# Optimization experiments

Hardware: AMD Instinct MI355X
Metric: run time of the kernel (lower is better)

The kernel has to match this reference:

```python
import jax, jax.numpy as jnp
import numpy as np

B, M, V, TOPK = 64, 8192, 128, 64
EPS = 1e-8  # stands in for LOG_EPS and F.cosine_similarity eps clamp


def setup_inputs() -> dict:
    key = jax.random.key(0)
    k1, k2 = jax.random.split(key)
    stdev = 1.0 / np.sqrt(M + V)
    memory = jax.random.uniform(k1, (B, M, V), dtype=jnp.float32, minval=-stdev, maxval=stdev)
    v = jax.random.normal(k2, (B, V), dtype=jnp.float32)
    return {"memory": memory, "v": v, "topk": TOPK}


def reference(memory, v, topk):
    # --- similarity(v, topk): cosine similarity of query against each memory slot ---
    a = memory + EPS                      # (B, M, V)
    b = v + EPS                           # (B, V)
    num = jnp.einsum('bmv,bv->bm', a, b)  # (B, M)
    denom = jnp.maximum(
        jnp.linalg.norm(a, axis=-1) * jnp.linalg.norm(b, axis=-1)[:, None], EPS
    )
    sim = num / denom                     # (B, M), unnormalized addressing weights
    # topk masking: torch zeroes the (M - topk) smallest entries via scatter_;
    # equivalently keep values >= the topk-th largest value (ties negligible for floats)
    kth = jax.lax.top_k(sim, topk)[0][:, -1:]   # (B, 1)
    w = jnp.where(sim >= kth, sim, jnp.zeros((), sim.dtype))
    # --- write(w, v): rank-1 outer-product update ---
    new_mem = memory + w[:, :, None] * v[:, None, :]   # (B, M, V)
    # --- read(w): weighted sum over slots; torch returns (B,1,1,V) via double unsqueeze ---
    read = jnp.einsum('bm,bmv->bv', w, new_mem)[:, None, None, :]
    return read
```

## Files before the change

### kernel.cpp

```cpp
#include <hip/hip_runtime.h>
#include <hip/hip_bf16.h>

#define B_DIM 64
#define M_DIM 8192
#define V_DIM 128
#define EPS 1e-8f
#define KCAP 2048

__global__ void sim_kernel(const float* __restrict__ mem,
                           const float* __restrict__ v,
                           float* __restrict__ sim) {
    const int b   = blockIdx.y;
    const int m0  = blockIdx.x * 32;
    const int tid = threadIdx.x;

    __shared__ float vs[V_DIM];
    __shared__ float s_bn;

    if (tid < V_DIM) vs[tid] = v[b * V_DIM + tid] + EPS;
    __syncthreads();

    if (tid < 32) {
        float s = 0.f;
#pragma unroll
        for (int j = 0; j < 4; ++j) { float x = vs[tid + 32 * j]; s += x * x; }
#pragma unroll
        for (int mk = 16; mk; mk >>= 1) s += __shfl_xor(s, mk, 32);
        if (tid == 0) s_bn = sqrtf(s);
    }
    __syncthreads();

    const int r    = tid >> 5;
    const int lane = tid & 31;
    const int c    = lane * 4;
    const float bn = s_bn;

#pragma unroll
    for (int rt = 0; rt < 4; ++rt) {
        const int m = m0 + rt * 8 + r;
        const float4* rowp =
            reinterpret_cast<const float4*>(mem + ((size_t)b * M_DIM + m) * V_DIM);
        float4 x = rowp[lane];
        float a0 = x.x + EPS, a1 = x.y + EPS, a2 = x.z + EPS, a3 = x.w + EPS;
        float dot = a0 * vs[c] + a1 * vs[c + 1] + a2 * vs[c + 2] + a3 * vs[c + 3];
        float ss  = a0 * a0 + a1 * a1 + a2 * a2 + a3 * a3;
#pragma unroll
        for (int mk = 16; mk; mk >>= 1) {
            dot += __shfl_xor(dot, mk, 32);
            ss  += __shfl_xor(ss,  mk, 32);
        }
        if (lane == 0) {
            float denom = fmaxf(sqrtf(ss) * bn, EPS);
            sim[(size_t)b * M_DIM + m] = dot / denom;
        }
    }
}

__device__ __forceinline__ unsigned int f2key(float f) {
    unsigned int u = __float_as_uint(f);
    return (u & 0x80000000u) ? ~u : (u | 0x80000000u);
}
__device__ __forceinline__ float key2f(unsigned int k) {
    return (k & 0x80000000u) ? __uint_as_float(k & 0x7FFFFFFFu)
                             : __uint_as_float(~k);
}

__global__ void topk_read_kernel(const float* __restrict__ mem,
                                 const float* __restrict__ v,
                                 const float* __restrict__ sim,
                                 const int* __restrict__ topk_p,
                                 float* __restrict__ out) {
    const int b   = blockIdx.x;
    const int tid = threadIdx.x;
    const int NT  = 256;

    __shared__ unsigned int keys[M_DIM];
    __shared__ unsigned int hist[256];
    __shared__ unsigned int s_prefix;
    __shared__ int s_k;
    __shared__ int s_cnt;
    __shared__ int   s_idx[KCAP];
    __shared__ float s_w[KCAP];
    __shared__ float s_sumw2;
    __shared__ float s_acc[256];

    for (int i = tid; i < M_DIM; i += NT)
        keys[i] = f2key(sim[(size_t)b * M_DIM + i]);
    if (tid == 0) { s_prefix = 0u; s_k = topk_p[0]; s_cnt = 0; }
    __syncthreads();

    for (int p = 3; p >= 0; --p) {
        hist[tid & 255] = 0u;
        __syncthreads();
        const unsigned int dm = (p == 3) ? 0u : (0xFFFFFFFFu << ((p + 1) * 8));
        const unsigned int pf = s_prefix;
        for (int i = tid; i < M_DIM; i += NT) {
            unsigned int ky = keys[i];
            if ((ky & dm) == pf)
                atomicAdd(&hist[(ky >> (p * 8)) & 0xFFu], 1u);
        }
        __syncthreads();
        if (tid == 0) {
            int k = s_k;
            for (int vq = 255; vq >= 0; --vq) {
                int c = (int)hist[vq];
                if (k <= c) {
                    s_prefix = pf | ((unsigned int)vq << (p * 8));
                    s_k = k;
                    break;
                }
                k -= c;
            }
        }
        __syncthreads();
    }
    const unsigned int kth = s_prefix;

    for (int i = tid; i < M_DIM; i += NT) {
        unsigned int ky = keys[i];
        if (ky >= kth) {
            int pos = atomicAdd(&s_cnt, 1);
            if (pos < KCAP) { s_idx[pos] = i; s_w[pos] = key2f(ky); }
        }
    }
    __syncthreads();
    const int cnt = min(s_cnt, KCAP);

    if (tid < 64) {
        float s = 0.f;
        for (int i = tid; i < cnt; i += 64) s += s_w[i] * s_w[i];
#pragma unroll
        for (int mk = 32; mk; mk >>= 1) s += __shfl_xor(s, mk, 64);
        if (tid == 0) s_sumw2 = s;
    }
    __syncthreads();

    const int col  = tid & 127;
    const int half = tid >> 7;
    float acc = 0.f;
    const float* mb = mem + (size_t)b * M_DIM * V_DIM;
    for (int j = half; j < cnt; j += 2)
        acc += s_w[j] * mb[(size_t)s_idx[j] * V_DIM + col];
    s_acc[tid] = acc;
    __syncthreads();
    if (tid < 128)
        out[b * V_DIM + tid] =
            s_acc[tid] + s_acc[tid + 128] + s_sumw2 * v[b * V_DIM + tid];
}

extern "C" void kernel_launch(void* const* d_in, const int* in_sizes, int n_in,
                              void* d_out, int out_size, void* d_ws, size_t ws_size,
                              hipStream_t stream) {
    const float* mem   = (const float*)d_in[0];
    const float* v     = (const float*)d_in[1];
    const int*   topk  = (const int*)d_in[2];
    float* out         = (float*)d_out;
    float* sim         = (float*)d_ws;

    dim3 grid1(M_DIM / 32, B_DIM);
    sim_kernel<<<grid1, 256, 0, stream>>>(mem, v, sim);

    topk_read_kernel<<<B_DIM, 256, 0, stream>>>(mem, v, sim, topk, out);
}
```

Measured before the change: 432.9 us.

## Rework similarity mapping and parallelize radix-select histogram and threshold scan

The similarity kernel now maps 16 lanes per row over 64 rows per block, uses rsqrt with a precomputed inverse query norm, and writes sortable keys directly. The top-k kernel uses per-wave privatized histograms and a parallel suffix scan in place of a serial single-thread bin search. The gather-read loop is unrolled with four independent accumulators to raise memory-level parallelism. The rsqrt and reciprocal change the rounding of the similarity slightly, and the denominator clamp is dropped, which could shift tie decisions at the k-th value.

```diff
diff --git a/kernel.cpp b/kernel.cpp
--- a/kernel.cpp
+++ b/kernel.cpp
@@ -6,55 +6,6 @@
 #define V_DIM 128
 #define EPS 1e-8f
 #define KCAP 2048
-
-__global__ void sim_kernel(const float* __restrict__ mem,
-                           const float* __restrict__ v,
-                           float* __restrict__ sim) {
-    const int b   = blockIdx.y;
-    const int m0  = blockIdx.x * 32;
-    const int tid = threadIdx.x;
-
-    __shared__ float vs[V_DIM];
-    __shared__ float s_bn;
-
-    if (tid < V_DIM) vs[tid] = v[b * V_DIM + tid] + EPS;
-    __syncthreads();
-
-    if (tid < 32) {
-        float s = 0.f;
-#pragma unroll
-        for (int j = 0; j < 4; ++j) { float x = vs[tid + 32 * j]; s += x * x; }
-#pragma unroll
-        for (int mk = 16; mk; mk >>= 1) s += __shfl_xor(s, mk, 32);
-        if (tid == 0) s_bn = sqrtf(s);
-    }
-    __syncthreads();
-
-    const int r    = tid >> 5;
-    const int lane = tid & 31;
-    const int c    = lane * 4;
-    const float bn = s_bn;
-
-#pragma unroll
-    for (int rt = 0; rt < 4; ++rt) {
-        const int m = m0 + rt * 8 + r;
-        const float4* rowp =
-            reinterpret_cast<const float4*>(mem + ((size_t)b * M_DIM + m) * V_DIM);
-        float4 x = rowp[lane];
-        float a0 = x.x + EPS, a1 = x.y + EPS, a2 = x.z + EPS, a3 = x.w + EPS;
-        float dot = a0 * vs[c] + a1 * vs[c + 1] + a2 * vs[c + 2] + a3 * vs[c + 3];
-        float ss  = a0 * a0 + a1 * a1 + a2 * a2 + a3 * a3;
-#pragma unroll
-        for (int mk = 16; mk; mk >>= 1) {
-            dot += __shfl_xor(dot, mk, 32);
-            ss  += __shfl_xor(ss,  mk, 32);
-        }
-        if (lane == 0) {
-            float denom = fmaxf(sqrtf(ss) * bn, EPS);
-            sim[(size_t)b * M_DIM + m] = dot / denom;
-        }
-    }
-}
 
 __device__ __forceinline__ unsigned int f2key(float f) {
     unsigned int u = __float_as_uint(f);
@@ -65,17 +16,74 @@
                              : __uint_as_float(~k);
 }
 
+__global__ void sim_kernel(const float* __restrict__ mem,
+                           const float* __restrict__ v,
+                           unsigned int* __restrict__ keys_out) {
+    const int b    = blockIdx.y;
+    const int m0   = blockIdx.x * 64;
+    const int tid  = threadIdx.x;
+    const int wave = tid >> 6;
+    const int lane = tid & 63;
+    const int rw   = lane >> 4;
+    const int sub  = lane & 15;
+
+    __shared__ float vs[V_DIM];
+    __shared__ float s_invbn;
+
+    if (tid < V_DIM) vs[tid] = v[b * V_DIM + tid] + EPS;
+    __syncthreads();
+
+    if (tid < 64) {
+        float x0 = vs[tid], x1 = vs[tid + 64];
+        float s = x0 * x0 + x1 * x1;
+#pragma unroll
+        for (int mk = 32; mk; mk >>= 1) s += __shfl_xor(s, mk, 64);
+        if (tid == 0) s_invbn = 1.0f / sqrtf(s);
+    }
+    __syncthreads();
+
+    const float4 va = *reinterpret_cast<const float4*>(&vs[sub * 4]);
+    const float4 vb = *reinterpret_cast<const float4*>(&vs[sub * 4 + 64]);
+    const float invbn = s_invbn;
+
+#pragma unroll
+    for (int t = 0; t < 4; ++t) {
+        const int m = m0 + t * 16 + wave * 4 + rw;
+        const float4* rp =
+            reinterpret_cast<const float4*>(mem + ((size_t)b * M_DIM + m) * V_DIM);
+        float4 x0 = rp[sub];
+        float4 x1 = rp[sub + 16];
+        float a0 = x0.x + EPS, a1 = x0.y + EPS, a2 = x0.z + EPS, a3 = x0.w + EPS;
+        float a4 = x1.x + EPS, a5 = x1.y + EPS, a6 = x1.z + EPS, a7 = x1.w + EPS;
+        float dot = a0 * va.x + a1 * va.y + a2 * va.z + a3 * va.w
+                  + a4 * vb.x + a5 * vb.y + a6 * vb.z + a7 * vb.w;
+        float ss  = a0 * a0 + a1 * a1 + a2 * a2 + a3 * a3
+                  + a4 * a4 + a5 * a5 + a6 * a6 + a7 * a7;
+#pragma unroll
+        for (int mk = 8; mk; mk >>= 1) {
+            dot += __shfl_xor(dot, mk, 16);
+            ss  += __shfl_xor(ss,  mk, 16);
+        }
+        if (sub == 0) {
+            float sim = dot * rsqrtf(ss) * invbn;
+            keys_out[(size_t)b * M_DIM + m] = f2key(sim);
+        }
+    }
+}
+
 __global__ void topk_read_kernel(const float* __restrict__ mem,
                                  const float* __restrict__ v,
-                                 const float* __restrict__ sim,
+                                 const unsigned int* __restrict__ keys_in,
                                  const int* __restrict__ topk_p,
                                  float* __restrict__ out) {
     const int b   = blockIdx.x;
     const int tid = threadIdx.x;
     const int NT  = 256;
+    const int wv  = tid >> 6;
 
     __shared__ unsigned int keys[M_DIM];
-    __shared__ unsigned int hist[256];
+    __shared__ unsigned int hist[4 * 256];
+    __shared__ int          sfx[256];
     __shared__ unsigned int s_prefix;
     __shared__ int s_k;
     __shared__ int s_cnt;
@@ -85,32 +93,38 @@
     __shared__ float s_acc[256];
 
     for (int i = tid; i < M_DIM; i += NT)
-        keys[i] = f2key(sim[(size_t)b * M_DIM + i]);
+        keys[i] = keys_in[(size_t)b * M_DIM + i];
     if (tid == 0) { s_prefix = 0u; s_k = topk_p[0]; s_cnt = 0; }
     __syncthreads();
 
     for (int p = 3; p >= 0; --p) {
-        hist[tid & 255] = 0u;
+#pragma unroll
+        for (int h = tid; h < 1024; h += NT) hist[h] = 0u;
         __syncthreads();
         const unsigned int dm = (p == 3) ? 0u : (0xFFFFFFFFu << ((p + 1) * 8));
         const unsigned int pf = s_prefix;
+        const int k_cur = s_k;
         for (int i = tid; i < M_DIM; i += NT) {
             unsigned int ky = keys[i];
             if ((ky & dm) == pf)
-                atomicAdd(&hist[(ky >> (p * 8)) & 0xFFu], 1u);
+                atomicAdd(&hist[wv * 256 + ((ky >> (p * 8)) & 0xFFu)], 1u);
         }
         __syncthreads();
-        if (tid == 0) {
-            int k = s_k;
-            for (int vq = 255; vq >= 0; --vq) {
-                int c = (int)hist[vq];
-                if (k <= c) {
-                    s_prefix = pf | ((unsigned int)vq << (p * 8));
-                    s_k = k;
-                    break;
-                }
-                k -= c;
-            }
+        int c = (int)(hist[tid] + hist[256 + tid] + hist[512 + tid] + hist[768 + tid]);
+        sfx[tid] = c;
+        __syncthreads();
+#pragma unroll
+        for (int off = 1; off < 256; off <<= 1) {
+            int x = (tid + off < 256) ? sfx[tid + off] : 0;
+            __syncthreads();
+            sfx[tid] += x;
+            __syncthreads();
+        }
+        int S_t  = sfx[tid];
+        int S_t1 = (tid < 255) ? sfx[tid + 1] : 0;
+        if (S_t >= k_cur && S_t1 < k_cur) {
+            s_prefix = pf | ((unsigned int)tid << (p * 8));
+            s_k = k_cur - S_t1;
         }
         __syncthreads();
     }
@@ -137,11 +151,18 @@
 
     const int col  = tid & 127;
     const int half = tid >> 7;
-    float acc = 0.f;
     const float* mb = mem + (size_t)b * M_DIM * V_DIM;
-    for (int j = half; j < cnt; j += 2)
-        acc += s_w[j] * mb[(size_t)s_idx[j] * V_DIM + col];
-    s_acc[tid] = acc;
+    float a0 = 0.f, a1 = 0.f, a2 = 0.f, a3 = 0.f;
+    int j = half;
+    for (; j + 6 < cnt; j += 8) {
+        a0 += s_w[j]     * mb[(size_t)s_idx[j]     * V_DIM + col];
+        a1 += s_w[j + 2] * mb[(size_t)s_idx[j + 2] * V_DIM + col];
+        a2 += s_w[j + 4] * mb[(size_t)s_idx[j + 4] * V_DIM + col];
+        a3 += s_w[j + 6] * mb[(size_t)s_idx[j + 6] * V_DIM + col];
+    }
+    for (; j < cnt; j += 2)
+        a0 += s_w[j] * mb[(size_t)s_idx[j] * V_DIM + col];
+    s_acc[tid] = (a0 + a1) + (a2 + a3);
     __syncthreads();
     if (tid < 128)
         out[b * V_DIM + tid] =
@@ -151,14 +172,14 @@
 extern "C" void kernel_launch(void* const* d_in, const int* in_sizes, int n_in,
                               void* d_out, int out_size, void* d_ws, size_t ws_size,
                               hipStream_t stream) {
-    const float* mem   = (const float*)d_in[0];
-    const float* v     = (const float*)d_in[1];
-    const int*   topk  = (const int*)d_in[2];
-    float* out         = (float*)d_out;
-    float* sim         = (float*)d_ws;
+    const float* mem  = (const float*)d_in[0];
+    const float* v    = (const float*)d_in[1];
+    const int*   topk = (const int*)d_in[2];
+    float* out        = (float*)d_out;
+    unsigned int* keys = (unsigned int*)d_ws;
 
-    dim3 grid1(M_DIM / 32, B_DIM);
-    sim_kernel<<<grid1, 256, 0, stream>>>(mem, v, sim);
+    dim3 grid1(M_DIM / 64, B_DIM);
+    sim_kernel<<<grid1, 256, 0, stream>>>(mem, v, keys);
 
-    topk_read_kernel<<<B_DIM, 256, 0, stream>>>(mem, v, sim, topk, out);
+    topk_read_kernel<<<B_DIM, 256, 0, stream>>>(mem, v, keys, topk, out);
 }
```

Result: faster. 378.7 us (-12.5%).
